# Optimization experiments

Hardware: AMD Instinct MI355X
Metric: run time of the kernel (lower is better)

The kernel has to match this reference:

```python
import jax, jax.numpy as jnp
import numpy as np

H = 1024
S = 65536


def setup_inputs() -> dict:
    key = jax.random.key(0)
    k1, k2, k3, k4 = jax.random.split(key, 4)
    hidden = jax.random.normal(k1, (H,), dtype=jnp.float32)
    encoder_outputs = jax.random.normal(k2, (S, H), dtype=jnp.float32)
    # nn.Linear(H, H) params, scaled like PyTorch default init (~1/sqrt(H))
    W = jax.random.normal(k3, (H, H), dtype=jnp.float32) / np.sqrt(H)
    b = jax.random.normal(k4, (H,), dtype=jnp.float32) / np.sqrt(H)
    return {"hidden": hidden, "encoder_outputs": encoder_outputs, "W": W, "b": b}


def reference(hidden, encoder_outputs, W, b):
    # Original per-timestep loop: scores[i] = hidden . (W @ enc[i] + b)
    # Fused batched form: enc @ (W^T @ hidden) + (b . hidden)  -- same math,
    # one streaming GEMV over the [S, H] encoder outputs instead of S launches.
    v = W.T @ hidden                      # [H]
    scores = encoder_outputs @ v + jnp.dot(b, hidden)  # [S]
    attn = jax.nn.softmax(scores)         # softmax over seq dim
    return attn[None, None, :]            # [1, 1, S]
```

## Files before the change

kernel.cpp:

```cpp
#include <hip/hip_runtime.h>

#define H 1024
#define S 65536

__global__ __launch_bounds__(256) void k_compute_v(const float* __restrict__ W,
                                                   const float* __restrict__ hidden,
                                                   float* __restrict__ v) {
    __shared__ float sh[H];
    const int t = threadIdx.x;
    for (int i = t; i < H; i += 256) sh[i] = hidden[i];
    __syncthreads();
    const int j = blockIdx.x * 256 + t;
    float a0 = 0.f, a1 = 0.f, a2 = 0.f, a3 = 0.f;
    for (int i = 0; i < H; i += 4) {
        a0 += W[(size_t)(i + 0) * H + j] * sh[i + 0];
        a1 += W[(size_t)(i + 1) * H + j] * sh[i + 1];
        a2 += W[(size_t)(i + 2) * H + j] * sh[i + 2];
        a3 += W[(size_t)(i + 3) * H + j] * sh[i + 3];
    }
    v[j] = (a0 + a1) + (a2 + a3);
}

__global__ __launch_bounds__(256) void k_scores(const float* __restrict__ enc,
                                                const float* __restrict__ v,
                                                float* __restrict__ scores,
                                                float* __restrict__ bmax) {
    const int lane = threadIdx.x & 63;
    const int warp = threadIdx.x >> 6;
    const float4* v4 = (const float4*)v;
    const float4 vr0 = v4[lane];
    const float4 vr1 = v4[lane + 64];
    const float4 vr2 = v4[lane + 128];
    const float4 vr3 = v4[lane + 192];

    const int wave_global = blockIdx.x * 4 + warp;
    const float4* e4 = (const float4*)enc;
    float wmax = -INFINITY;

    for (int it = 0; it < 16; ++it) {
        const int row = wave_global + it * 4096;
        const float4* e = e4 + (size_t)row * 256;
        const float4 a0 = e[lane];
        const float4 a1 = e[lane + 64];
        const float4 a2 = e[lane + 128];
        const float4 a3 = e[lane + 192];
        float acc = a0.x * vr0.x + a0.y * vr0.y + a0.z * vr0.z + a0.w * vr0.w
                  + a1.x * vr1.x + a1.y * vr1.y + a1.z * vr1.z + a1.w * vr1.w
                  + a2.x * vr2.x + a2.y * vr2.y + a2.z * vr2.z + a2.w * vr2.w
                  + a3.x * vr3.x + a3.y * vr3.y + a3.z * vr3.z + a3.w * vr3.w;
        #pragma unroll
        for (int m = 1; m < 64; m <<= 1) acc += __shfl_xor(acc, m, 64);
        if (lane == 0) scores[row] = acc;
        wmax = fmaxf(wmax, acc);
    }

    __shared__ float smax[4];
    if (lane == 0) smax[warp] = wmax;
    __syncthreads();
    if (threadIdx.x == 0)
        bmax[blockIdx.x] = fmaxf(fmaxf(smax[0], smax[1]), fmaxf(smax[2], smax[3]));
}

__global__ __launch_bounds__(256) void k_exp(const float* __restrict__ scores,
                                             const float* __restrict__ bmax,
                                             float* __restrict__ out,
                                             float* __restrict__ bsum) {
    const int t = threadIdx.x;
    const int lane = t & 63;
    const int warp = t >> 6;

    float m = fmaxf(fmaxf(bmax[t], bmax[t + 256]),
                    fmaxf(bmax[t + 512], bmax[t + 768]));
    #pragma unroll
    for (int d = 1; d < 64; d <<= 1) m = fmaxf(m, __shfl_xor(m, d, 64));
    __shared__ float sm[4];
    if (lane == 0) sm[warp] = m;
    __syncthreads();
    const float gmax = fmaxf(fmaxf(sm[0], sm[1]), fmaxf(sm[2], sm[3]));

    const int i = blockIdx.x * 256 + t;
    const float e = __expf(scores[i] - gmax);
    out[i] = e;

    float s = e;
    #pragma unroll
    for (int d = 1; d < 64; d <<= 1) s += __shfl_xor(s, d, 64);
    __shared__ float ss[4];
    if (lane == 0) ss[warp] = s;
    __syncthreads();
    if (t == 0) bsum[blockIdx.x] = (ss[0] + ss[1]) + (ss[2] + ss[3]);
}

__global__ __launch_bounds__(256) void k_norm(const float* __restrict__ bsum,
                                              float* __restrict__ out) {
    const int t = threadIdx.x;
    const int lane = t & 63;
    const int warp = t >> 6;

    float s = bsum[t];
    #pragma unroll
    for (int d = 1; d < 64; d <<= 1) s += __shfl_xor(s, d, 64);
    __shared__ float ss[4];
    if (lane == 0) ss[warp] = s;
    __syncthreads();
    const float inv = 1.0f / ((ss[0] + ss[1]) + (ss[2] + ss[3]));

    const int i = blockIdx.x * 256 + t;
    out[i] *= inv;
}

extern "C" void kernel_launch(void* const* d_in, const int* in_sizes, int n_in,
                              void* d_out, int out_size, void* d_ws, size_t ws_size,
                              hipStream_t stream) {
    const float* hidden = (const float*)d_in[0];
    const float* enc    = (const float*)d_in[1];
    const float* W      = (const float*)d_in[2];
    float* out = (float*)d_out;

    float* v      = (float*)d_ws;
    float* scores = v + 1024;
    float* bmax   = scores + S;
    float* bsum   = bmax + 1024;

    k_compute_v<<<4,    256, 0, stream>>>(W, hidden, v);
    k_scores   <<<1024, 256, 0, stream>>>(enc, v, scores, bmax);
    k_exp      <<<256,  256, 0, stream>>>(scores, bmax, out, bsum);
    k_norm     <<<256,  256, 0, stream>>>(bsum, out);
}
```

Baseline: 408.7 us.

## Split W^T·hidden GEMV into 128-block partial sums plus reduction kernel

The W^T @ hidden computation previously ran on only 4 blocks, each thread walking all 1024 rows serially. It is now split across 128 blocks, each summing 8 rows with float4 loads into a partial buffer in workspace, followed by a small kernel that reduces the 128 partials. This spreads the 4 MB read of W over many CUs at the cost of one extra launch and a 512 KB partial write and read.

```diff
diff --git a/kernel.cpp b/kernel.cpp
--- a/kernel.cpp
+++ b/kernel.cpp
@@ -3,22 +3,33 @@
 #define H 1024
 #define S 65536
 
-__global__ __launch_bounds__(256) void k_compute_v(const float* __restrict__ W,
+__global__ __launch_bounds__(256) void k1a_partial(const float* __restrict__ W,
                                                    const float* __restrict__ hidden,
-                                                   float* __restrict__ v) {
-    __shared__ float sh[H];
+                                                   float* __restrict__ partial) {
     const int t = threadIdx.x;
-    for (int i = t; i < H; i += 256) sh[i] = hidden[i];
-    __syncthreads();
-    const int j = blockIdx.x * 256 + t;
-    float a0 = 0.f, a1 = 0.f, a2 = 0.f, a3 = 0.f;
-    for (int i = 0; i < H; i += 4) {
-        a0 += W[(size_t)(i + 0) * H + j] * sh[i + 0];
-        a1 += W[(size_t)(i + 1) * H + j] * sh[i + 1];
-        a2 += W[(size_t)(i + 2) * H + j] * sh[i + 2];
-        a3 += W[(size_t)(i + 3) * H + j] * sh[i + 3];
+    const int b = blockIdx.x;
+    const int i0 = b * 8;
+    const float4* W4 = (const float4*)W;
+    float4 acc = make_float4(0.f, 0.f, 0.f, 0.f);
+    #pragma unroll
+    for (int r = 0; r < 8; ++r) {
+        const float hv = hidden[i0 + r];
+        const float4 w = W4[(size_t)(i0 + r) * 256 + t];
+        acc.x += w.x * hv; acc.y += w.y * hv;
+        acc.z += w.z * hv; acc.w += w.w * hv;
     }
-    v[j] = (a0 + a1) + (a2 + a3);
+    ((float4*)partial)[(size_t)b * 256 + t] = acc;
+}
+
+__global__ __launch_bounds__(256) void k1b_reduce(const float* __restrict__ partial,
+                                                  float* __restrict__ v) {
+    const int j = blockIdx.x * 256 + threadIdx.x;
+    float s0 = 0.f, s1 = 0.f;
+    for (int b = 0; b < 128; b += 2) {
+        s0 += partial[(size_t)b * H + j];
+        s1 += partial[(size_t)(b + 1) * H + j];
+    }
+    v[j] = s0 + s1;
 }
 
 __global__ __launch_bounds__(256) void k_scores(const float* __restrict__ enc,
@@ -117,12 +128,14 @@
     const float* W      = (const float*)d_in[2];
     float* out = (float*)d_out;
 
-    float* v      = (float*)d_ws;
-    float* scores = v + 1024;
-    float* bmax   = scores + S;
-    float* bsum   = bmax + 1024;
+    float* v       = (float*)d_ws;
+    float* scores  = v + 1024;
+    float* bmax    = scores + S;
+    float* bsum    = bmax + 1024;
+    float* partial = bsum + 256;
 
-    k_compute_v<<<4,    256, 0, stream>>>(W, hidden, v);
+    k1a_partial<<<128,  256, 0, stream>>>(W, hidden, partial);
+    k1b_reduce <<<4,    256, 0, stream>>>(partial, v);
     k_scores   <<<1024, 256, 0, stream>>>(enc, v, scores, bmax);
     k_exp      <<<256,  256, 0, stream>>>(scores, bmax, out, bsum);
     k_norm     <<<256,  256, 0, stream>>>(bsum, out);
```

Measured after the change: 384.6 us. -5.9%, faster.
